# Kernel tuning notes

Measured on AMD Instinct MI355X. Metric: run time of the kernel, lower is better.

The kernel has to match this reference:

```python
import jax, jax.numpy as jnp
import numpy as np

B, T, E = 32, 2048, 128

def setup_inputs() -> dict:
    key = jax.random.key(0)
    ks = jax.random.split(key, 6)
    return {
        "x1": jax.random.normal(ks[0], (B, T, E), dtype=jnp.float32),
        "x2": jax.random.normal(ks[1], (B, T, E), dtype=jnp.float32),
        "W1": jax.random.normal(ks[2], (E, 1), dtype=jnp.float32) * 0.05,
        "b1": jnp.zeros((T, 1), dtype=jnp.float32),
        "U1": jax.random.normal(ks[3], (E, T), dtype=jnp.float32) * 0.05,
        "W2": jax.random.normal(ks[4], (E, 1), dtype=jnp.float32) * 0.05,
        "b2": jnp.zeros((T, 1), dtype=jnp.float32),
        "U2": jax.random.normal(ks[5], (E, T), dtype=jnp.float32) * 0.05,
    }


def reference(x1, x2, W1, b1, U1, W2, b2, U2):
    # S[b,i,j] = <x1[b,i], x2[b,j]>  -> (B, T, T)
    S = jnp.einsum('bie,bje->bij', x1, x2)
    inv_T = jnp.float32(1.0) / S.shape[1]
    # c1 = mean_j sum_i S[b,i,j] * x2[b,i,e]  -> (B, E)
    c1 = jnp.einsum('bij,bie->be', S, x2) * inv_T
    # c2 = mean_i sum_j S[b,i,j] * x1[b,j,e]  -> (B, E)
    c2 = jnp.einsum('bij,bje->be', S, x1) * inv_T
    # attention logits: (B, T)
    et1 = c1 @ U1 + jnp.squeeze(x1 @ W1 + b1, axis=-1)
    et2 = c2 @ U2 + jnp.squeeze(x2 @ W2 + b2, axis=-1)
    at1 = jax.nn.softmax(et1, axis=-1)
    at2 = jax.nn.softmax(et2, axis=-1)
    # attention-weighted sums: (B, E)
    o1 = jnp.einsum('bt,bte->be', at1, x1)
    o2 = jnp.einsum('bt,bte->be', at2, x2)
    # merge_mode == 'concat'
    return jnp.concatenate([o1, o2], axis=1)
```

## Files before the change

kernel.cpp:

```cpp
#include <hip/hip_runtime.h>


#define B_ 32
#define T_ 2048
#define E_ 128
#define EV (E_/4)
#define INV_T (1.0f/2048.0f)

#define WS_PSX1 0
#define WS_PSX2 (B_*16*E_)
#define WS_PC1  (2*B_*16*E_)
#define WS_PC2  (2*B_*16*E_ + B_*32*E_)
#define WS_ET1  (2*B_*16*E_ + 2*B_*32*E_)
#define WS_ET2  (WS_ET1 + B_*T_)

__device__ __forceinline__ float dot4(float4 a, float4 b) {
    return a.x*b.x + a.y*b.y + a.z*b.z + a.w*b.w;
}
__device__ __forceinline__ void fma4(float4& a, float s, const float4 v) {
    a.x += s*v.x; a.y += s*v.y; a.z += s*v.z; a.w += s*v.w;
}
__device__ __forceinline__ void add4(float4& a, const float4 v) {
    a.x += v.x; a.y += v.y; a.z += v.z; a.w += v.w;
}

__global__ __launch_bounds__(256)
void k1_psx(const float* __restrict__ x1, const float* __restrict__ x2,
            float* __restrict__ ws) {
    __shared__ float4 s_r1[256], s_r2[256];
    const int b = blockIdx.x, g = blockIdx.y, tid = threadIdx.x;
    const float4* p1 = (const float4*)x1 + ((size_t)b*T_ + g*128)*EV;
    const float4* p2 = (const float4*)x2 + ((size_t)b*T_ + g*128)*EV;
    const int rg = tid >> 5, q = tid & 31;
    float4 a1 = {0,0,0,0}, a2 = {0,0,0,0};
    #pragma unroll
    for (int i = 0; i < 16; ++i) {
        int r = i*8 + rg;
        add4(a1, p1[r*EV + q]);
        add4(a2, p2[r*EV + q]);
    }
    s_r1[tid] = a1; s_r2[tid] = a2;
    __syncthreads();
    for (int s = 128; s >= 32; s >>= 1) {
        if (tid < s) { add4(s_r1[tid], s_r1[tid+s]); add4(s_r2[tid], s_r2[tid+s]); }
        __syncthreads();
    }
    if (tid < 32) {
        ((float4*)(ws + WS_PSX1))[(b*16 + g)*EV + tid] = s_r1[tid];
        ((float4*)(ws + WS_PSX2))[(b*16 + g)*EV + tid] = s_r2[tid];
    }
}

__global__ __launch_bounds__(256)
void k2_wc(const float* __restrict__ x1, const float* __restrict__ x2,
           const float* __restrict__ W1, const float* __restrict__ b1,
           const float* __restrict__ W2, const float* __restrict__ b2,
           float* __restrict__ ws) {
    __shared__ float4 s_r1[256], s_r2[256];
    __shared__ float  s_a[E_], s_b[E_], s_wa[E_], s_wb[E_];
    __shared__ float  s_w1[64], s_w2[64];
    const int b = blockIdx.x, ch = blockIdx.y, tid = threadIdx.x;
    if (tid < E_) {
        float sa = 0.f, sb = 0.f;
        #pragma unroll
        for (int g = 0; g < 16; ++g) {
            sa += ws[WS_PSX1 + (b*16 + g)*E_ + tid];
            sb += ws[WS_PSX2 + (b*16 + g)*E_ + tid];
        }
        s_a[tid] = sa;
        s_b[tid] = sb;
        s_wa[tid] = W1[tid];
        s_wb[tid] = W2[tid];
    }
    __syncthreads();
    const float4* p1 = (const float4*)x1 + ((size_t)b*T_ + ch*64)*EV;
    const float4* p2 = (const float4*)x2 + ((size_t)b*T_ + ch*64)*EV;
    const float4* sx1v = (const float4*)s_a;
    const float4* sx2v = (const float4*)s_b;
    const float4* W1v  = (const float4*)s_wa;
    const float4* W2v  = (const float4*)s_wb;
    const int rowoff = tid >> 5, q = tid & 31;

    float4 v1[8], v2[8];
    #pragma unroll
    for (int i = 0; i < 8; ++i) {
        int r = i*8 + rowoff;
        v1[i] = p1[r*EV + q];
        v2[i] = p2[r*EV + q];
    }

    float* et1 = ws + WS_ET1 + (size_t)b*T_ + ch*64;
    float* et2 = ws + WS_ET2 + (size_t)b*T_ + ch*64;
    #pragma unroll
    for (int i = 0; i < 8; ++i) {
        int r = i*8 + rowoff;
        float pw1 = dot4(v1[i], sx2v[q]);
        float px1 = dot4(v1[i], W1v[q]);
        float pw2 = dot4(v2[i], sx1v[q]);
        float px2 = dot4(v2[i], W2v[q]);
        #pragma unroll
        for (int m = 1; m <= 16; m <<= 1) {
            pw1 += __shfl_xor(pw1, m);
            px1 += __shfl_xor(px1, m);
            pw2 += __shfl_xor(pw2, m);
            px2 += __shfl_xor(px2, m);
        }
        if (q == 0) {
            s_w1[r] = pw1; s_w2[r] = pw2;
            int trow = ch*64 + r;
            et1[r] = px1 + b1[trow];
            et2[r] = px2 + b2[trow];
        }
    }
    __syncthreads();

    float4 a1 = {0,0,0,0}, a2 = {0,0,0,0};
    #pragma unroll
    for (int i = 0; i < 8; ++i) {
        int r = i*8 + rowoff;
        fma4(a1, s_w1[r], v2[i]);
        fma4(a2, s_w2[r], v1[i]);
    }
    s_r1[tid] = a1; s_r2[tid] = a2;
    __syncthreads();
    for (int s = 128; s >= 32; s >>= 1) {
        if (tid < s) { add4(s_r1[tid], s_r1[tid+s]); add4(s_r2[tid], s_r2[tid+s]); }
        __syncthreads();
    }
    if (tid < 32) {
        float4 t1 = s_r1[tid], t2 = s_r2[tid];
        t1.x *= INV_T; t1.y *= INV_T; t1.z *= INV_T; t1.w *= INV_T;
        t2.x *= INV_T; t2.y *= INV_T; t2.z *= INV_T; t2.w *= INV_T;
        ((float4*)(ws + WS_PC1))[(b*32 + ch)*EV + tid] = t1;
        ((float4*)(ws + WS_PC2))[(b*32 + ch)*EV + tid] = t2;
    }
}

__global__ __launch_bounds__(512)
void k3_et_softmax(const float* __restrict__ U1, const float* __restrict__ U2,
                   float* __restrict__ ws, float* __restrict__ out) {
    __shared__ float s_c[E_];
    __shared__ float red[512];
    const int b = blockIdx.x, sel = blockIdx.y, tid = threadIdx.x;
    const float* U = sel ? U2 : U1;
    const float* pc = ws + (sel ? WS_PC2 : WS_PC1);
    float4* et4 = (float4*)(ws + (sel ? WS_ET2 : WS_ET1) + (size_t)b*T_);
    if (tid < E_) {
        float s = 0.f;
        #pragma unroll
        for (int ch = 0; ch < 32; ++ch) s += pc[(b*32 + ch)*E_ + tid];
        s_c[tid] = s;
    } else if (tid >= 256 && tid < 256 + E_) {
        out[b*2*E_ + sel*E_ + (tid - 256)] = 0.f;
    }
    __syncthreads();
    const float4* U4 = (const float4*)U;
    float4 acc = et4[tid];
    #pragma unroll 4
    for (int e = 0; e < E_; ++e) {
        fma4(acc, s_c[e], U4[(size_t)e*(T_/4) + tid]);
    }
    float m = fmaxf(fmaxf(acc.x, acc.y), fmaxf(acc.z, acc.w));
    red[tid] = m; __syncthreads();
    for (int s = 256; s > 0; s >>= 1) {
        if (tid < s) red[tid] = fmaxf(red[tid], red[tid+s]);
        __syncthreads();
    }
    m = red[0]; __syncthreads();
    float4 e4;
    e4.x = __expf(acc.x - m); e4.y = __expf(acc.y - m);
    e4.z = __expf(acc.z - m); e4.w = __expf(acc.w - m);
    red[tid] = e4.x + e4.y + e4.z + e4.w;
    __syncthreads();
    for (int s = 256; s > 0; s >>= 1) {
        if (tid < s) red[tid] += red[tid+s];
        __syncthreads();
    }
    float il = 1.f / red[0];
    e4.x *= il; e4.y *= il; e4.z *= il; e4.w *= il;
    et4[tid] = e4;
}

__global__ __launch_bounds__(256)
void k5_out(const float* __restrict__ x1, const float* __restrict__ x2,
            const float* __restrict__ ws, float* __restrict__ out) {
    __shared__ float4 s_r1[256], s_r2[256];
    __shared__ float s_p1[128], s_p2[128];
    const int b = blockIdx.x, g = blockIdx.y, tid = threadIdx.x;
    const float* pr1 = ws + WS_ET1 + (size_t)b*T_ + g*128;
    const float* pr2 = ws + WS_ET2 + (size_t)b*T_ + g*128;
    if (tid < 128)  s_p1[tid] = pr1[tid];
    else            s_p2[tid - 128] = pr2[tid - 128];
    __syncthreads();
    const float4* p1 = (const float4*)x1 + ((size_t)b*T_ + g*128)*EV;
    const float4* p2 = (const float4*)x2 + ((size_t)b*T_ + g*128)*EV;
    const int rg = tid >> 5, q = tid & 31;
    float4 a1 = {0,0,0,0}, a2 = {0,0,0,0};
    #pragma unroll
    for (int i = 0; i < 16; ++i) {
        int r = i*8 + rg;
        fma4(a1, s_p1[r], p1[r*EV + q]);
        fma4(a2, s_p2[r], p2[r*EV + q]);
    }
    s_r1[tid] = a1; s_r2[tid] = a2;
    __syncthreads();
    for (int s = 128; s >= 32; s >>= 1) {
        if (tid < s) { add4(s_r1[tid], s_r1[tid+s]); add4(s_r2[tid], s_r2[tid+s]); }
        __syncthreads();
    }
    if (tid < 32) {
        float4 t1 = s_r1[tid], t2 = s_r2[tid];
        atomicAdd(&out[b*2*E_ + tid*4+0], t1.x);
        atomicAdd(&out[b*2*E_ + tid*4+1], t1.y);
        atomicAdd(&out[b*2*E_ + tid*4+2], t1.z);
        atomicAdd(&out[b*2*E_ + tid*4+3], t1.w);
        atomicAdd(&out[b*2*E_ + E_ + tid*4+0], t2.x);
        atomicAdd(&out[b*2*E_ + E_ + tid*4+1], t2.y);
        atomicAdd(&out[b*2*E_ + E_ + tid*4+2], t2.z);
        atomicAdd(&out[b*2*E_ + E_ + tid*4+3], t2.w);
    }
}

extern "C" void kernel_launch(void* const* d_in, const int* in_sizes, int n_in,
                              void* d_out, int out_size, void* d_ws, size_t ws_size,
                              hipStream_t stream) {
    const float* x1 = (const float*)d_in[0];
    const float* x2 = (const float*)d_in[1];
    const float* W1 = (const float*)d_in[2];
    const float* b1 = (const float*)d_in[3];
    const float* U1 = (const float*)d_in[4];
    const float* W2 = (const float*)d_in[5];
    const float* b2 = (const float*)d_in[6];
    const float* U2 = (const float*)d_in[7];
    float* ws  = (float*)d_ws;
    float* out = (float*)d_out;

    k1_psx<<<dim3(B_, 16), 256, 0, stream>>>(x1, x2, ws);
    k2_wc<<<dim3(B_, 32), 256, 0, stream>>>(x1, x2, W1, b1, W2, b2, ws);
    k3_et_softmax<<<dim3(B_, 2), 512, 0, stream>>>(U1, U2, ws, out);
    k5_out<<<dim3(B_, 16), 256, 0, stream>>>(x1, x2, ws, out);
}
```

Before: 148.9 us.

## Fuse four stages into one cooperative kernel with grid-wide syncs

The four kernel launches are replaced by a single cooperative kernel of 512 blocks that uses grid.sync between phases. The x·W projection is moved into the first pass, and the c1/c2 partial reductions now use 16 chunks per batch instead of 32. The goal is to remove launch gaps and improve cache reuse of x1/x2 across phases. In exchange, each grid barrier costs something, and the softmax phase runs on only 64 of the blocks while the rest sit idle. The original four-kernel path is kept as a fallback if the cooperative launch fails.

After: 336.2 us. +125.7%, slower.

```diff
diff --git a/kernel.cpp b/kernel.cpp
--- a/kernel.cpp
+++ b/kernel.cpp
@@ -1,4 +1,7 @@
 #include <hip/hip_runtime.h>
+#include <hip/hip_cooperative_groups.h>
+
+namespace cg = cooperative_groups;
 
 
 #define B_ 32
@@ -22,6 +25,191 @@
 }
 __device__ __forceinline__ void add4(float4& a, const float4 v) {
     a.x += v.x; a.y += v.y; a.z += v.z; a.w += v.w;
+}
+__device__ __forceinline__ float bfly32(float v) {
+    #pragma unroll
+    for (int m = 1; m <= 16; m <<= 1) v += __shfl_xor(v, m);
+    return v;
+}
+
+__global__ __launch_bounds__(256, 2)
+void fused(const float* __restrict__ x1, const float* __restrict__ x2,
+           const float* __restrict__ W1, const float* __restrict__ b1,
+           const float* __restrict__ U1, const float* __restrict__ W2,
+           const float* __restrict__ b2, const float* __restrict__ U2,
+           float* __restrict__ ws, float* __restrict__ out)
+{
+    __shared__ float4 s_r1[256], s_r2[256];
+    __shared__ float  s_a[E_], s_b[E_];
+    __shared__ float  s_wa[E_], s_wb[E_];
+    __shared__ float  s_p1[128], s_p2[128];
+    cg::grid_group grid = cg::this_grid();
+    const int tid = threadIdx.x, bid = blockIdx.x;
+    const int b = bid >> 4, g = bid & 15;
+    const int rg = tid >> 5, q = tid & 31;
+
+    if (tid < 128) s_wa[tid] = W1[tid];
+    else           s_wb[tid - 128] = W2[tid - 128];
+    __syncthreads();
+
+    const float4* p1 = (const float4*)x1 + ((size_t)b*T_ + g*128)*EV;
+    const float4* p2 = (const float4*)x2 + ((size_t)b*T_ + g*128)*EV;
+    const float4* W1v = (const float4*)s_wa;
+    const float4* W2v = (const float4*)s_wb;
+    float* et1g = ws + WS_ET1 + (size_t)b*T_ + g*128;
+    float* et2g = ws + WS_ET2 + (size_t)b*T_ + g*128;
+
+    {
+        float4 a1 = {0,0,0,0}, a2 = {0,0,0,0};
+        #pragma unroll
+        for (int i = 0; i < 16; ++i) {
+            int r = i*8 + rg;
+            float4 v1 = p1[r*EV + q];
+            float4 v2 = p2[r*EV + q];
+            add4(a1, v1); add4(a2, v2);
+            float d1 = bfly32(dot4(v1, W1v[q]));
+            float d2 = bfly32(dot4(v2, W2v[q]));
+            if (q == 0) {
+                int trow = g*128 + r;
+                et1g[r] = d1 + b1[trow];
+                et2g[r] = d2 + b2[trow];
+            }
+        }
+        s_r1[tid] = a1; s_r2[tid] = a2;
+        __syncthreads();
+        for (int s = 128; s >= 32; s >>= 1) {
+            if (tid < s) { add4(s_r1[tid], s_r1[tid+s]); add4(s_r2[tid], s_r2[tid+s]); }
+            __syncthreads();
+        }
+        if (tid < 32) {
+            ((float4*)(ws + WS_PSX1))[(b*16 + g)*EV + tid] = s_r1[tid];
+            ((float4*)(ws + WS_PSX2))[(b*16 + g)*EV + tid] = s_r2[tid];
+        }
+        if (g == 0) out[b*2*E_ + tid] = 0.f;
+    }
+    grid.sync();
+
+    {
+        if (tid < 128) {
+            float s = 0.f;
+            #pragma unroll
+            for (int gg = 0; gg < 16; ++gg) s += ws[WS_PSX1 + (b*16 + gg)*E_ + tid];
+            s_a[tid] = s;
+        } else {
+            float s = 0.f;
+            #pragma unroll
+            for (int gg = 0; gg < 16; ++gg) s += ws[WS_PSX2 + (b*16 + gg)*E_ + (tid-128)];
+            s_b[tid - 128] = s;
+        }
+        __syncthreads();
+        const float4* sx1v = (const float4*)s_a;
+        const float4* sx2v = (const float4*)s_b;
+        float4 a1 = {0,0,0,0}, a2 = {0,0,0,0};
+        #pragma unroll
+        for (int i = 0; i < 16; ++i) {
+            int r = i*8 + rg;
+            float4 v1 = p1[r*EV + q];
+            float4 v2 = p2[r*EV + q];
+            float w1r = bfly32(dot4(v1, sx2v[q]));
+            float w2r = bfly32(dot4(v2, sx1v[q]));
+            fma4(a1, w1r, v2);
+            fma4(a2, w2r, v1);
+        }
+        __syncthreads();
+        s_r1[tid] = a1; s_r2[tid] = a2;
+        __syncthreads();
+        for (int s = 128; s >= 32; s >>= 1) {
+            if (tid < s) { add4(s_r1[tid], s_r1[tid+s]); add4(s_r2[tid], s_r2[tid+s]); }
+            __syncthreads();
+        }
+        if (tid < 32) {
+            float4 t1 = s_r1[tid], t2 = s_r2[tid];
+            t1.x *= INV_T; t1.y *= INV_T; t1.z *= INV_T; t1.w *= INV_T;
+            t2.x *= INV_T; t2.y *= INV_T; t2.z *= INV_T; t2.w *= INV_T;
+            ((float4*)(ws + WS_PC1))[(b*16 + g)*EV + tid] = t1;
+            ((float4*)(ws + WS_PC2))[(b*16 + g)*EV + tid] = t2;
+        }
+    }
+    grid.sync();
+
+    if (bid < 2*B_) {
+        const int pb = bid >> 1, sel = bid & 1;
+        const float* U  = sel ? U2 : U1;
+        const float* pc = ws + (sel ? WS_PC2 : WS_PC1);
+        float4* et4 = (float4*)(ws + (sel ? WS_ET2 : WS_ET1) + (size_t)pb*T_);
+        if (tid < 128) {
+            float s = 0.f;
+            #pragma unroll
+            for (int gg = 0; gg < 16; ++gg) s += pc[(pb*16 + gg)*E_ + tid];
+            s_a[tid] = s;
+        }
+        __syncthreads();
+        const float4* U4 = (const float4*)U;
+        float4 acc0 = et4[tid];
+        float4 acc1 = et4[tid + 256];
+        #pragma unroll 4
+        for (int e = 0; e < E_; ++e) {
+            float ce = s_a[e];
+            fma4(acc0, ce, U4[(size_t)e*(T_/4) + tid]);
+            fma4(acc1, ce, U4[(size_t)e*(T_/4) + tid + 256]);
+        }
+        float* red = (float*)s_r1;
+        float m = fmaxf(fmaxf(fmaxf(acc0.x, acc0.y), fmaxf(acc0.z, acc0.w)),
+                        fmaxf(fmaxf(acc1.x, acc1.y), fmaxf(acc1.z, acc1.w)));
+        red[tid] = m; __syncthreads();
+        for (int s = 128; s > 0; s >>= 1) {
+            if (tid < s) red[tid] = fmaxf(red[tid], red[tid+s]);
+            __syncthreads();
+        }
+        m = red[0]; __syncthreads();
+        float4 e0, e1;
+        e0.x = __expf(acc0.x - m); e0.y = __expf(acc0.y - m);
+        e0.z = __expf(acc0.z - m); e0.w = __expf(acc0.w - m);
+        e1.x = __expf(acc1.x - m); e1.y = __expf(acc1.y - m);
+        e1.z = __expf(acc1.z - m); e1.w = __expf(acc1.w - m);
+        red[tid] = e0.x + e0.y + e0.z + e0.w + e1.x + e1.y + e1.z + e1.w;
+        __syncthreads();
+        for (int s = 128; s > 0; s >>= 1) {
+            if (tid < s) red[tid] += red[tid+s];
+            __syncthreads();
+        }
+        float il = 1.f / red[0];
+        e0.x *= il; e0.y *= il; e0.z *= il; e0.w *= il;
+        e1.x *= il; e1.y *= il; e1.z *= il; e1.w *= il;
+        et4[tid]       = e0;
+        et4[tid + 256] = e1;
+    }
+    grid.sync();
+
+    {
+        if (tid < 128) s_p1[tid] = et1g[tid];
+        else           s_p2[tid - 128] = et2g[tid - 128];
+        __syncthreads();
+        float4 a1 = {0,0,0,0}, a2 = {0,0,0,0};
+        #pragma unroll
+        for (int i = 0; i < 16; ++i) {
+            int r = i*8 + rg;
+            fma4(a1, s_p1[r], p1[r*EV + q]);
+            fma4(a2, s_p2[r], p2[r*EV + q]);
+        }
+        s_r1[tid] = a1; s_r2[tid] = a2;
+        __syncthreads();
+        for (int s = 128; s >= 32; s >>= 1) {
+            if (tid < s) { add4(s_r1[tid], s_r1[tid+s]); add4(s_r2[tid], s_r2[tid+s]); }
+            __syncthreads();
+        }
+        if (tid < 32) {
+            float4 t1 = s_r1[tid], t2 = s_r2[tid];
+            atomicAdd(&out[b*2*E_ + tid*4+0], t1.x);
+            atomicAdd(&out[b*2*E_ + tid*4+1], t1.y);
+            atomicAdd(&out[b*2*E_ + tid*4+2], t1.z);
+            atomicAdd(&out[b*2*E_ + tid*4+3], t1.w);
+            atomicAdd(&out[b*2*E_ + E_ + tid*4+0], t2.x);
+            atomicAdd(&out[b*2*E_ + E_ + tid*4+1], t2.y);
+            atomicAdd(&out[b*2*E_ + E_ + tid*4+2], t2.z);
+            atomicAdd(&out[b*2*E_ + E_ + tid*4+3], t2.w);
+        }
+    }
 }
 
 __global__ __launch_bounds__(256)
@@ -58,7 +246,6 @@
            float* __restrict__ ws) {
     __shared__ float4 s_r1[256], s_r2[256];
     __shared__ float  s_a[E_], s_b[E_], s_wa[E_], s_wb[E_];
-    __shared__ float  s_w1[64], s_w2[64];
     const int b = blockIdx.x, ch = blockIdx.y, tid = threadIdx.x;
     if (tid < E_) {
         float sa = 0.f, sb = 0.f;
@@ -67,10 +254,8 @@
             sa += ws[WS_PSX1 + (b*16 + g)*E_ + tid];
             sb += ws[WS_PSX2 + (b*16 + g)*E_ + tid];
         }
-        s_a[tid] = sa;
-        s_b[tid] = sb;
-        s_wa[tid] = W1[tid];
-        s_wb[tid] = W2[tid];
+        s_a[tid] = sa; s_b[tid] = sb;
+        s_wa[tid] = W1[tid]; s_wb[tid] = W2[tid];
     }
     __syncthreads();
     const float4* p1 = (const float4*)x1 + ((size_t)b*T_ + ch*64)*EV;
@@ -80,46 +265,25 @@
     const float4* W1v  = (const float4*)s_wa;
     const float4* W2v  = (const float4*)s_wb;
     const int rowoff = tid >> 5, q = tid & 31;
-
-    float4 v1[8], v2[8];
-    #pragma unroll
-    for (int i = 0; i < 8; ++i) {
-        int r = i*8 + rowoff;
-        v1[i] = p1[r*EV + q];
-        v2[i] = p2[r*EV + q];
-    }
-
     float* et1 = ws + WS_ET1 + (size_t)b*T_ + ch*64;
     float* et2 = ws + WS_ET2 + (size_t)b*T_ + ch*64;
-    #pragma unroll
-    for (int i = 0; i < 8; ++i) {
-        int r = i*8 + rowoff;
-        float pw1 = dot4(v1[i], sx2v[q]);
-        float px1 = dot4(v1[i], W1v[q]);
-        float pw2 = dot4(v2[i], sx1v[q]);
-        float px2 = dot4(v2[i], W2v[q]);
-        #pragma unroll
-        for (int m = 1; m <= 16; m <<= 1) {
-            pw1 += __shfl_xor(pw1, m);
-            px1 += __shfl_xor(px1, m);
-            pw2 += __shfl_xor(pw2, m);
-            px2 += __shfl_xor(px2, m);
-        }
-        if (q == 0) {
-            s_w1[r] = pw1; s_w2[r] = pw2;
-            int trow = ch*64 + r;
-            et1[r] = px1 + b1[trow];
-            et2[r] = px2 + b2[trow];
-        }
-    }
-    __syncthreads();
-
     float4 a1 = {0,0,0,0}, a2 = {0,0,0,0};
     #pragma unroll
     for (int i = 0; i < 8; ++i) {
         int r = i*8 + rowoff;
-        fma4(a1, s_w1[r], v2[i]);
-        fma4(a2, s_w2[r], v1[i]);
+        float4 v1 = p1[r*EV + q];
+        float4 v2 = p2[r*EV + q];
+        float pw1 = bfly32(dot4(v1, sx2v[q]));
+        float px1 = bfly32(dot4(v1, W1v[q]));
+        float pw2 = bfly32(dot4(v2, sx1v[q]));
+        float px2 = bfly32(dot4(v2, W2v[q]));
+        if (q == 0) {
+            int trow = ch*64 + r;
+            et1[r] = px1 + b1[trow];
+            et2[r] = px2 + b2[trow];
+        }
+        fma4(a1, pw1, v2);
+        fma4(a2, pw2, v1);
     }
     s_r1[tid] = a1; s_r2[tid] = a2;
     __syncthreads();
@@ -157,9 +321,7 @@
     const float4* U4 = (const float4*)U;
     float4 acc = et4[tid];
     #pragma unroll 4
-    for (int e = 0; e < E_; ++e) {
-        fma4(acc, s_c[e], U4[(size_t)e*(T_/4) + tid]);
-    }
+    for (int e = 0; e < E_; ++e) fma4(acc, s_c[e], U4[(size_t)e*(T_/4) + tid]);
     float m = fmaxf(fmaxf(acc.x, acc.y), fmaxf(acc.z, acc.w));
     red[tid] = m; __syncthreads();
     for (int s = 256; s > 0; s >>= 1) {
@@ -189,8 +351,8 @@
     const int b = blockIdx.x, g = blockIdx.y, tid = threadIdx.x;
     const float* pr1 = ws + WS_ET1 + (size_t)b*T_ + g*128;
     const float* pr2 = ws + WS_ET2 + (size_t)b*T_ + g*128;
-    if (tid < 128)  s_p1[tid] = pr1[tid];
-    else            s_p2[tid - 128] = pr2[tid - 128];
+    if (tid < 128) s_p1[tid] = pr1[tid];
+    else           s_p2[tid - 128] = pr2[tid - 128];
     __syncthreads();
     const float4* p1 = (const float4*)x1 + ((size_t)b*T_ + g*128)*EV;
     const float4* p2 = (const float4*)x2 + ((size_t)b*T_ + g*128)*EV;
@@ -235,8 +397,15 @@
     float* ws  = (float*)d_ws;
     float* out = (float*)d_out;
 
-    k1_psx<<<dim3(B_, 16), 256, 0, stream>>>(x1, x2, ws);
-    k2_wc<<<dim3(B_, 32), 256, 0, stream>>>(x1, x2, W1, b1, W2, b2, ws);
-    k3_et_softmax<<<dim3(B_, 2), 512, 0, stream>>>(U1, U2, ws, out);
-    k5_out<<<dim3(B_, 16), 256, 0, stream>>>(x1, x2, ws, out);
-}
+    void* args[] = { (void*)&x1, (void*)&x2, (void*)&W1, (void*)&b1, (void*)&U1,
+                     (void*)&W2, (void*)&b2, (void*)&U2, (void*)&ws, (void*)&out };
+    hipError_t err = hipLaunchCooperativeKernel((void*)fused, dim3(512), dim3(256),
+                                                args, 0, stream);
+    if (err != hipSuccess) {
+        (void)hipGetLastError();
+        k1_psx<<<dim3(B_, 16), 256, 0, stream>>>(x1, x2, ws);
+        k2_wc<<<dim3(B_, 32), 256, 0, stream>>>(x1, x2, W1, b1, W2, b2, ws);
+        k3_et_softmax<<<dim3(B_, 2), 512, 0, stream>>>(U1, U2, ws, out);
+        k5_out<<<dim3(B_, 16), 256, 0, stream>>>(x1, x2, ws, out);
+    }
+}
```

## Move x·W logits into first pass, stream k2 over 128-row tiles, split k3 accumulators

Applied to the files above, without the earlier changes.

Computes the x·W + b logit terms in the first reduction kernel, which already reads every row of x1/x2, so k2 no longer needs them. k2 now processes 128-row tiles with 16 blocks per batch and streams each row, fusing the butterfly-reduced weight directly into the accumulation without a shared-memory round trip. k3 splits the U-projection into four independent accumulators to break the FMA dependency chain. The change trades away k2 parallelism (half the blocks) and adds shuffle work to k1 in exchange for fewer syncs and smaller partial buffers.

After: 158.9 us. 1.07x slower.

```diff
diff --git a/kernel.cpp b/kernel.cpp
--- a/kernel.cpp
+++ b/kernel.cpp
@@ -10,8 +10,8 @@
 #define WS_PSX1 0
 #define WS_PSX2 (B_*16*E_)
 #define WS_PC1  (2*B_*16*E_)
-#define WS_PC2  (2*B_*16*E_ + B_*32*E_)
-#define WS_ET1  (2*B_*16*E_ + 2*B_*32*E_)
+#define WS_PC2  (3*B_*16*E_)
+#define WS_ET1  (4*B_*16*E_)
 #define WS_ET2  (WS_ET1 + B_*T_)
 
 __device__ __forceinline__ float dot4(float4 a, float4 b) {
@@ -23,21 +23,44 @@
 __device__ __forceinline__ void add4(float4& a, const float4 v) {
     a.x += v.x; a.y += v.y; a.z += v.z; a.w += v.w;
 }
+__device__ __forceinline__ float bfly32(float v) {
+    #pragma unroll
+    for (int m = 1; m <= 16; m <<= 1) v += __shfl_xor(v, m);
+    return v;
+}
 
 __global__ __launch_bounds__(256)
-void k1_psx(const float* __restrict__ x1, const float* __restrict__ x2,
-            float* __restrict__ ws) {
+void k1_psx_et(const float* __restrict__ x1, const float* __restrict__ x2,
+               const float* __restrict__ W1, const float* __restrict__ b1,
+               const float* __restrict__ W2, const float* __restrict__ b2,
+               float* __restrict__ ws) {
     __shared__ float4 s_r1[256], s_r2[256];
+    __shared__ float  s_wa[E_], s_wb[E_];
     const int b = blockIdx.x, g = blockIdx.y, tid = threadIdx.x;
+    if (tid < 128) s_wa[tid] = W1[tid];
+    else           s_wb[tid - 128] = W2[tid - 128];
+    __syncthreads();
     const float4* p1 = (const float4*)x1 + ((size_t)b*T_ + g*128)*EV;
     const float4* p2 = (const float4*)x2 + ((size_t)b*T_ + g*128)*EV;
+    const float4* W1v = (const float4*)s_wa;
+    const float4* W2v = (const float4*)s_wb;
+    float* et1g = ws + WS_ET1 + (size_t)b*T_ + g*128;
+    float* et2g = ws + WS_ET2 + (size_t)b*T_ + g*128;
     const int rg = tid >> 5, q = tid & 31;
     float4 a1 = {0,0,0,0}, a2 = {0,0,0,0};
     #pragma unroll
     for (int i = 0; i < 16; ++i) {
         int r = i*8 + rg;
-        add4(a1, p1[r*EV + q]);
-        add4(a2, p2[r*EV + q]);
+        float4 v1 = p1[r*EV + q];
+        float4 v2 = p2[r*EV + q];
+        add4(a1, v1); add4(a2, v2);
+        float d1 = bfly32(dot4(v1, W1v[q]));
+        float d2 = bfly32(dot4(v2, W2v[q]));
+        if (q == 0) {
+            int trow = g*128 + r;
+            et1g[r] = d1 + b1[trow];
+            et2g[r] = d2 + b2[trow];
+        }
     }
     s_r1[tid] = a1; s_r2[tid] = a2;
     __syncthreads();
@@ -53,73 +76,37 @@
 
 __global__ __launch_bounds__(256)
 void k2_wc(const float* __restrict__ x1, const float* __restrict__ x2,
-           const float* __restrict__ W1, const float* __restrict__ b1,
-           const float* __restrict__ W2, const float* __restrict__ b2,
            float* __restrict__ ws) {
     __shared__ float4 s_r1[256], s_r2[256];
-    __shared__ float  s_a[E_], s_b[E_], s_wa[E_], s_wb[E_];
-    __shared__ float  s_w1[64], s_w2[64];
-    const int b = blockIdx.x, ch = blockIdx.y, tid = threadIdx.x;
-    if (tid < E_) {
-        float sa = 0.f, sb = 0.f;
+    __shared__ float  s_a[E_], s_b[E_];
+    const int b = blockIdx.x, g = blockIdx.y, tid = threadIdx.x;
+    if (tid < 128) {
+        float s = 0.f;
         #pragma unroll
-        for (int g = 0; g < 16; ++g) {
-            sa += ws[WS_PSX1 + (b*16 + g)*E_ + tid];
-            sb += ws[WS_PSX2 + (b*16 + g)*E_ + tid];
-        }
-        s_a[tid] = sa;
-        s_b[tid] = sb;
-        s_wa[tid] = W1[tid];
-        s_wb[tid] = W2[tid];
-    }
-    __syncthreads();
-    const float4* p1 = (const float4*)x1 + ((size_t)b*T_ + ch*64)*EV;
-    const float4* p2 = (const float4*)x2 + ((size_t)b*T_ + ch*64)*EV;
+        for (int gg = 0; gg < 16; ++gg) s += ws[WS_PSX1 + (b*16 + gg)*E_ + tid];
+        s_a[tid] = s;
+    } else {
+        float s = 0.f;
+        #pragma unroll
+        for (int gg = 0; gg < 16; ++gg) s += ws[WS_PSX2 + (b*16 + gg)*E_ + (tid-128)];
+        s_b[tid - 128] = s;
+    }
+    __syncthreads();
+    const float4* p1 = (const float4*)x1 + ((size_t)b*T_ + g*128)*EV;
+    const float4* p2 = (const float4*)x2 + ((size_t)b*T_ + g*128)*EV;
     const float4* sx1v = (const float4*)s_a;
     const float4* sx2v = (const float4*)s_b;
-    const float4* W1v  = (const float4*)s_wa;
-    const float4* W2v  = (const float4*)s_wb;
-    const int rowoff = tid >> 5, q = tid & 31;
-
-    float4 v1[8], v2[8];
-    #pragma unroll
-    for (int i = 0; i < 8; ++i) {
-        int r = i*8 + rowoff;
-        v1[i] = p1[r*EV + q];
-        v2[i] = p2[r*EV + q];
-    }
-
-    float* et1 = ws + WS_ET1 + (size_t)b*T_ + ch*64;
-    float* et2 = ws + WS_ET2 + (size_t)b*T_ + ch*64;
-    #pragma unroll
-    for (int i = 0; i < 8; ++i) {
-        int r = i*8 + rowoff;
-        float pw1 = dot4(v1[i], sx2v[q]);
-        float px1 = dot4(v1[i], W1v[q]);
-        float pw2 = dot4(v2[i], sx1v[q]);
-        float px2 = dot4(v2[i], W2v[q]);
-        #pragma unroll
-        for (int m = 1; m <= 16; m <<= 1) {
-            pw1 += __shfl_xor(pw1, m);
-            px1 += __shfl_xor(px1, m);
-            pw2 += __shfl_xor(pw2, m);
-            px2 += __shfl_xor(px2, m);
-        }
-        if (q == 0) {
-            s_w1[r] = pw1; s_w2[r] = pw2;
-            int trow = ch*64 + r;
-            et1[r] = px1 + b1[trow];
-            et2[r] = px2 + b2[trow];
-        }
-    }
-    __syncthreads();
-
+    const int rg = tid >> 5, q = tid & 31;
     float4 a1 = {0,0,0,0}, a2 = {0,0,0,0};
     #pragma unroll
-    for (int i = 0; i < 8; ++i) {
-        int r = i*8 + rowoff;
-        fma4(a1, s_w1[r], v2[i]);
-        fma4(a2, s_w2[r], v1[i]);
+    for (int i = 0; i < 16; ++i) {
+        int r = i*8 + rg;
+        float4 v1 = p1[r*EV + q];
+        float4 v2 = p2[r*EV + q];
+        float w1r = bfly32(dot4(v1, sx2v[q]));
+        float w2r = bfly32(dot4(v2, sx1v[q]));
+        fma4(a1, w1r, v2);
+        fma4(a2, w2r, v1);
     }
     s_r1[tid] = a1; s_r2[tid] = a2;
     __syncthreads();
@@ -131,8 +118,8 @@
         float4 t1 = s_r1[tid], t2 = s_r2[tid];
         t1.x *= INV_T; t1.y *= INV_T; t1.z *= INV_T; t1.w *= INV_T;
         t2.x *= INV_T; t2.y *= INV_T; t2.z *= INV_T; t2.w *= INV_T;
-        ((float4*)(ws + WS_PC1))[(b*32 + ch)*EV + tid] = t1;
-        ((float4*)(ws + WS_PC2))[(b*32 + ch)*EV + tid] = t2;
+        ((float4*)(ws + WS_PC1))[(b*16 + g)*EV + tid] = t1;
+        ((float4*)(ws + WS_PC2))[(b*16 + g)*EV + tid] = t2;
     }
 }
 
@@ -148,19 +135,24 @@
     if (tid < E_) {
         float s = 0.f;
         #pragma unroll
-        for (int ch = 0; ch < 32; ++ch) s += pc[(b*32 + ch)*E_ + tid];
+        for (int gg = 0; gg < 16; ++gg) s += pc[(b*16 + gg)*E_ + tid];
         s_c[tid] = s;
     } else if (tid >= 256 && tid < 256 + E_) {
         out[b*2*E_ + sel*E_ + (tid - 256)] = 0.f;
     }
     __syncthreads();
     const float4* U4 = (const float4*)U;
-    float4 acc = et4[tid];
-    #pragma unroll 4
-    for (int e = 0; e < E_; ++e) {
-        fma4(acc, s_c[e], U4[(size_t)e*(T_/4) + tid]);
-    }
-    float m = fmaxf(fmaxf(acc.x, acc.y), fmaxf(acc.z, acc.w));
+    float4 accA = et4[tid];
+    float4 accB = {0,0,0,0}, accC = {0,0,0,0}, accD = {0,0,0,0};
+    #pragma unroll 2
+    for (int e = 0; e < E_; e += 4) {
+        fma4(accA, s_c[e+0], U4[(size_t)(e+0)*(T_/4) + tid]);
+        fma4(accB, s_c[e+1], U4[(size_t)(e+1)*(T_/4) + tid]);
+        fma4(accC, s_c[e+2], U4[(size_t)(e+2)*(T_/4) + tid]);
+        fma4(accD, s_c[e+3], U4[(size_t)(e+3)*(T_/4) + tid]);
+    }
+    add4(accA, accB); add4(accC, accD); add4(accA, accC);
+    float m = fmaxf(fmaxf(accA.x, accA.y), fmaxf(accA.z, accA.w));
     red[tid] = m; __syncthreads();
     for (int s = 256; s > 0; s >>= 1) {
         if (tid < s) red[tid] = fmaxf(red[tid], red[tid+s]);
@@ -168,8 +160,8 @@
     }
     m = red[0]; __syncthreads();
     float4 e4;
-    e4.x = __expf(acc.x - m); e4.y = __expf(acc.y - m);
-    e4.z = __expf(acc.z - m); e4.w = __expf(acc.w - m);
+    e4.x = __expf(accA.x - m); e4.y = __expf(accA.y - m);
+    e4.z = __expf(accA.z - m); e4.w = __expf(accA.w - m);
     red[tid] = e4.x + e4.y + e4.z + e4.w;
     __syncthreads();
     for (int s = 256; s > 0; s >>= 1) {
@@ -189,8 +181,8 @@
     const int b = blockIdx.x, g = blockIdx.y, tid = threadIdx.x;
     const float* pr1 = ws + WS_ET1 + (size_t)b*T_ + g*128;
     const float* pr2 = ws + WS_ET2 + (size_t)b*T_ + g*128;
-    if (tid < 128)  s_p1[tid] = pr1[tid];
-    else            s_p2[tid - 128] = pr2[tid - 128];
+    if (tid < 128) s_p1[tid] = pr1[tid];
+    else           s_p2[tid - 128] = pr2[tid - 128];
     __syncthreads();
     const float4* p1 = (const float4*)x1 + ((size_t)b*T_ + g*128)*EV;
     const float4* p2 = (const float4*)x2 + ((size_t)b*T_ + g*128)*EV;
@@ -235,8 +227,8 @@
     float* ws  = (float*)d_ws;
     float* out = (float*)d_out;
 
-    k1_psx<<<dim3(B_, 16), 256, 0, stream>>>(x1, x2, ws);
-    k2_wc<<<dim3(B_, 32), 256, 0, stream>>>(x1, x2, W1, b1, W2, b2, ws);
+    k1_psx_et<<<dim3(B_, 16), 256, 0, stream>>>(x1, x2, W1, b1, W2, b2, ws);
+    k2_wc<<<dim3(B_, 16), 256, 0, stream>>>(x1, x2, ws);
     k3_et_softmax<<<dim3(B_, 2), 512, 0, stream>>>(U1, U2, ws, out);
     k5_out<<<dim3(B_, 16), 256, 0, stream>>>(x1, x2, ws, out);
 }
```

## Fuse logits/softmax stage into wc kernel via last-block ticket counter

Applied to the files above, without the earlier changes.

Removes the separate et/softmax kernel launch by having the last of the 32 blocks per batch (chosen with an atomic ticket counter and threadfences) reduce the partial c vectors and run the U matvec and softmax for both branches. Output zeroing and counter reset move to the first kernel. This saves one launch and its dependency gap. The cost is that the tail work now runs in only 32 blocks of 256 threads doing both branches serially, where before it ran in 64 blocks of 512 threads.

Result: slower. 229.1 us (+53.8%).

```diff
diff --git a/kernel.cpp b/kernel.cpp
--- a/kernel.cpp
+++ b/kernel.cpp
@@ -13,6 +13,7 @@
 #define WS_PC2  (2*B_*16*E_ + B_*32*E_)
 #define WS_ET1  (2*B_*16*E_ + 2*B_*32*E_)
 #define WS_ET2  (WS_ET1 + B_*T_)
+#define WS_CNT  (WS_ET2 + B_*T_)
 
 __device__ __forceinline__ float dot4(float4 a, float4 b) {
     return a.x*b.x + a.y*b.y + a.z*b.z + a.w*b.w;
@@ -23,10 +24,15 @@
 __device__ __forceinline__ void add4(float4& a, const float4 v) {
     a.x += v.x; a.y += v.y; a.z += v.z; a.w += v.w;
 }
+__device__ __forceinline__ float bfly32(float v) {
+    #pragma unroll
+    for (int m = 1; m <= 16; m <<= 1) v += __shfl_xor(v, m);
+    return v;
+}
 
 __global__ __launch_bounds__(256)
 void k1_psx(const float* __restrict__ x1, const float* __restrict__ x2,
-            float* __restrict__ ws) {
+            float* __restrict__ ws, float* __restrict__ out) {
     __shared__ float4 s_r1[256], s_r2[256];
     const int b = blockIdx.x, g = blockIdx.y, tid = threadIdx.x;
     const float4* p1 = (const float4*)x1 + ((size_t)b*T_ + g*128)*EV;
@@ -49,16 +55,22 @@
         ((float4*)(ws + WS_PSX1))[(b*16 + g)*EV + tid] = s_r1[tid];
         ((float4*)(ws + WS_PSX2))[(b*16 + g)*EV + tid] = s_r2[tid];
     }
+    if (g == 0) {
+        out[b*2*E_ + tid] = 0.f;
+        if (tid == 0) ((int*)(ws + WS_CNT))[b] = 0;
+    }
 }
 
 __global__ __launch_bounds__(256)
-void k2_wc(const float* __restrict__ x1, const float* __restrict__ x2,
-           const float* __restrict__ W1, const float* __restrict__ b1,
-           const float* __restrict__ W2, const float* __restrict__ b2,
-           float* __restrict__ ws) {
+void k2_wc_et(const float* __restrict__ x1, const float* __restrict__ x2,
+              const float* __restrict__ W1, const float* __restrict__ b1,
+              const float* __restrict__ U1, const float* __restrict__ W2,
+              const float* __restrict__ b2, const float* __restrict__ U2,
+              float* __restrict__ ws, float* __restrict__ out) {
     __shared__ float4 s_r1[256], s_r2[256];
     __shared__ float  s_a[E_], s_b[E_], s_wa[E_], s_wb[E_];
     __shared__ float  s_w1[64], s_w2[64];
+    __shared__ int    s_ticket;
     const int b = blockIdx.x, ch = blockIdx.y, tid = threadIdx.x;
     if (tid < E_) {
         float sa = 0.f, sb = 0.f;
@@ -67,10 +79,8 @@
             sa += ws[WS_PSX1 + (b*16 + g)*E_ + tid];
             sb += ws[WS_PSX2 + (b*16 + g)*E_ + tid];
         }
-        s_a[tid] = sa;
-        s_b[tid] = sb;
-        s_wa[tid] = W1[tid];
-        s_wb[tid] = W2[tid];
+        s_a[tid] = sa; s_b[tid] = sb;
+        s_wa[tid] = W1[tid]; s_wb[tid] = W2[tid];
     }
     __syncthreads();
     const float4* p1 = (const float4*)x1 + ((size_t)b*T_ + ch*64)*EV;
@@ -94,17 +104,10 @@
     #pragma unroll
     for (int i = 0; i < 8; ++i) {
         int r = i*8 + rowoff;
-        float pw1 = dot4(v1[i], sx2v[q]);
-        float px1 = dot4(v1[i], W1v[q]);
-        float pw2 = dot4(v2[i], sx1v[q]);
-        float px2 = dot4(v2[i], W2v[q]);
-        #pragma unroll
-        for (int m = 1; m <= 16; m <<= 1) {
-            pw1 += __shfl_xor(pw1, m);
-            px1 += __shfl_xor(px1, m);
-            pw2 += __shfl_xor(pw2, m);
-            px2 += __shfl_xor(px2, m);
-        }
+        float pw1 = bfly32(dot4(v1[i], sx2v[q]));
+        float px1 = bfly32(dot4(v1[i], W1v[q]));
+        float pw2 = bfly32(dot4(v2[i], sx1v[q]));
+        float px2 = bfly32(dot4(v2[i], W2v[q]));
         if (q == 0) {
             s_w1[r] = pw1; s_w2[r] = pw2;
             int trow = ch*64 + r;
@@ -134,51 +137,70 @@
         ((float4*)(ws + WS_PC1))[(b*32 + ch)*EV + tid] = t1;
         ((float4*)(ws + WS_PC2))[(b*32 + ch)*EV + tid] = t2;
     }
-}
-
-__global__ __launch_bounds__(512)
-void k3_et_softmax(const float* __restrict__ U1, const float* __restrict__ U2,
-                   float* __restrict__ ws, float* __restrict__ out) {
-    __shared__ float s_c[E_];
-    __shared__ float red[512];
-    const int b = blockIdx.x, sel = blockIdx.y, tid = threadIdx.x;
-    const float* U = sel ? U2 : U1;
-    const float* pc = ws + (sel ? WS_PC2 : WS_PC1);
-    float4* et4 = (float4*)(ws + (sel ? WS_ET2 : WS_ET1) + (size_t)b*T_);
-    if (tid < E_) {
+
+    __threadfence();
+    __syncthreads();
+    if (tid == 0) s_ticket = atomicAdd(&((int*)(ws + WS_CNT))[b], 1);
+    __syncthreads();
+    if (s_ticket != 31) return;
+    __threadfence();
+
+    if (tid < 128) {
         float s = 0.f;
         #pragma unroll
-        for (int ch = 0; ch < 32; ++ch) s += pc[(b*32 + ch)*E_ + tid];
-        s_c[tid] = s;
-    } else if (tid >= 256 && tid < 256 + E_) {
-        out[b*2*E_ + sel*E_ + (tid - 256)] = 0.f;
-    }
-    __syncthreads();
-    const float4* U4 = (const float4*)U;
-    float4 acc = et4[tid];
-    #pragma unroll 4
-    for (int e = 0; e < E_; ++e) {
-        fma4(acc, s_c[e], U4[(size_t)e*(T_/4) + tid]);
-    }
-    float m = fmaxf(fmaxf(acc.x, acc.y), fmaxf(acc.z, acc.w));
-    red[tid] = m; __syncthreads();
-    for (int s = 256; s > 0; s >>= 1) {
-        if (tid < s) red[tid] = fmaxf(red[tid], red[tid+s]);
-        __syncthreads();
-    }
-    m = red[0]; __syncthreads();
-    float4 e4;
-    e4.x = __expf(acc.x - m); e4.y = __expf(acc.y - m);
-    e4.z = __expf(acc.z - m); e4.w = __expf(acc.w - m);
-    red[tid] = e4.x + e4.y + e4.z + e4.w;
-    __syncthreads();
-    for (int s = 256; s > 0; s >>= 1) {
-        if (tid < s) red[tid] += red[tid+s];
-        __syncthreads();
-    }
-    float il = 1.f / red[0];
-    e4.x *= il; e4.y *= il; e4.z *= il; e4.w *= il;
-    et4[tid] = e4;
+        for (int cc = 0; cc < 32; ++cc) s += ws[WS_PC1 + (b*32 + cc)*E_ + tid];
+        s_a[tid] = s;
+    } else {
+        float s = 0.f;
+        #pragma unroll
+        for (int cc = 0; cc < 32; ++cc) s += ws[WS_PC2 + (b*32 + cc)*E_ + (tid-128)];
+        s_b[tid - 128] = s;
+    }
+    __syncthreads();
+
+    float* red = (float*)s_r1;
+    #pragma unroll
+    for (int sel = 0; sel < 2; ++sel) {
+        const float4* U4 = (const float4*)(sel ? U2 : U1);
+        const float*  cv = sel ? s_b : s_a;
+        float4* et4 = (float4*)(ws + (sel ? WS_ET2 : WS_ET1) + (size_t)b*T_);
+        float4 a0 = et4[tid], a1t = et4[tid + 256];
+        float4 b0 = {0,0,0,0}, b1t = {0,0,0,0};
+        #pragma unroll 4
+        for (int e = 0; e < E_; e += 2) {
+            float c0 = cv[e], c1 = cv[e+1];
+            fma4(a0,  c0, U4[(size_t)(e  )*(T_/4) + tid]);
+            fma4(a1t, c0, U4[(size_t)(e  )*(T_/4) + tid + 256]);
+            fma4(b0,  c1, U4[(size_t)(e+1)*(T_/4) + tid]);
+            fma4(b1t, c1, U4[(size_t)(e+1)*(T_/4) + tid + 256]);
+        }
+        add4(a0, b0); add4(a1t, b1t);
+        float m = fmaxf(fmaxf(fmaxf(a0.x, a0.y),  fmaxf(a0.z, a0.w)),
+                        fmaxf(fmaxf(a1t.x, a1t.y), fmaxf(a1t.z, a1t.w)));
+        red[tid] = m; __syncthreads();
+        for (int s = 128; s > 0; s >>= 1) {
+            if (tid < s) red[tid] = fmaxf(red[tid], red[tid+s]);
+            __syncthreads();
+        }
+        m = red[0]; __syncthreads();
+        float4 e0, e1;
+        e0.x = __expf(a0.x - m);  e0.y = __expf(a0.y - m);
+        e0.z = __expf(a0.z - m);  e0.w = __expf(a0.w - m);
+        e1.x = __expf(a1t.x - m); e1.y = __expf(a1t.y - m);
+        e1.z = __expf(a1t.z - m); e1.w = __expf(a1t.w - m);
+        red[tid] = e0.x + e0.y + e0.z + e0.w + e1.x + e1.y + e1.z + e1.w;
+        __syncthreads();
+        for (int s = 128; s > 0; s >>= 1) {
+            if (tid < s) red[tid] += red[tid+s];
+            __syncthreads();
+        }
+        float il = 1.f / red[0];
+        e0.x *= il; e0.y *= il; e0.z *= il; e0.w *= il;
+        e1.x *= il; e1.y *= il; e1.z *= il; e1.w *= il;
+        et4[tid]       = e0;
+        et4[tid + 256] = e1;
+        __syncthreads();
+    }
 }
 
 __global__ __launch_bounds__(256)
@@ -189,8 +211,8 @@
     const int b = blockIdx.x, g = blockIdx.y, tid = threadIdx.x;
     const float* pr1 = ws + WS_ET1 + (size_t)b*T_ + g*128;
     const float* pr2 = ws + WS_ET2 + (size_t)b*T_ + g*128;
-    if (tid < 128)  s_p1[tid] = pr1[tid];
-    else            s_p2[tid - 128] = pr2[tid - 128];
+    if (tid < 128) s_p1[tid] = pr1[tid];
+    else           s_p2[tid - 128] = pr2[tid - 128];
     __syncthreads();
     const float4* p1 = (const float4*)x1 + ((size_t)b*T_ + g*128)*EV;
     const float4* p2 = (const float4*)x2 + ((size_t)b*T_ + g*128)*EV;
@@ -235,8 +257,7 @@
     float* ws  = (float*)d_ws;
     float* out = (float*)d_out;
 
-    k1_psx<<<dim3(B_, 16), 256, 0, stream>>>(x1, x2, ws);
-    k2_wc<<<dim3(B_, 32), 256, 0, stream>>>(x1, x2, W1, b1, W2, b2, ws);
-    k3_et_softmax<<<dim3(B_, 2), 512, 0, stream>>>(U1, U2, ws, out);
+    k1_psx<<<dim3(B_, 16), 256, 0, stream>>>(x1, x2, ws, out);
+    k2_wc_et<<<dim3(B_, 32), 256, 0, stream>>>(x1, x2, W1, b1, U1, W2, b2, U2, ws, out);
     k5_out<<<dim3(B_, 16), 256, 0, stream>>>(x1, x2, ws, out);
 }
```
